# Kernel optimization log

Hardware: AMD Instinct MI355X
Metric: run time of the kernel (lower is better)

## Reference

```python
import jax, jax.numpy as jnp
import numpy as np

N_NODES = 50000
N_EDGES = 800000
IN_CH = 128
HEADS = 4
OUT_CH = 4
N_GRAPHS = 64
NEG_SLOPE = 0.2  # GATv2Conv default leaky_relu slope
EPS = 1e-5       # GraphNorm eps


def _seg_sum(x, seg, n):
    return jax.ops.segment_sum(x, seg, num_segments=n)


def _seg_mean(x, seg, n):
    s = _seg_sum(x, seg, n)
    cnt = _seg_sum(jnp.ones((seg.shape[0],), x.dtype), seg, n)
    return s / jnp.maximum(cnt, 1.0)[:, None]


def gatv2_conv(x, src, dst, n, w_l, w_r, att, bias, heads, out_ch, concat):
    # x: [N, F_in]; src/dst: [E_tot] (self-loops already appended)
    x_l = (x @ w_l).reshape(n, heads, out_ch)
    x_r = (x @ w_r).reshape(n, heads, out_ch)
    m = jax.nn.leaky_relu(x_l[src] + x_r[dst], NEG_SLOPE)   # [E, H, C]
    e = jnp.einsum('ehc,hc->eh', m, att)                    # [E, H]
    # softmax over incoming edges of each destination node
    e_max = jax.ops.segment_max(e, dst, num_segments=n)     # [N, H]
    w = jnp.exp(e - e_max[dst])
    denom = _seg_sum(w, dst, n)                             # [N, H]
    alpha = w / denom[dst]
    out = _seg_sum(alpha[:, :, None] * x_l[src], dst, n)    # [N, H, C]
    out = out.reshape(n, heads * out_ch) if concat else out.mean(axis=1)
    return out + bias


def graph_norm(x, batch, weight, bias, mean_scale, n_graphs):
    mu = _seg_mean(x, batch, n_graphs)                      # [G, C]
    out = x - mu[batch] * mean_scale
    var = _seg_mean(out * out, batch, n_graphs)
    return out / jnp.sqrt(var[batch] + EPS) * weight + bias


def setup_inputs() -> dict:
    key = jax.random.key(0)
    ks = jax.random.split(key, 20)
    H = HEADS
    d = {}
    d['x'] = jax.random.normal(ks[0], (N_NODES, IN_CH), dtype=jnp.float32)
    d['edge_index'] = jax.random.randint(ks[1], (2, N_EDGES), 0, N_NODES, dtype=jnp.int32)
    d['batch'] = jnp.sort(jax.random.randint(ks[2], (N_NODES,), 0, N_GRAPHS, dtype=jnp.int32))
    def glorot(k, shape):
        fan = shape[0] + shape[-1]
        return jax.random.normal(k, shape, dtype=jnp.float32) * np.sqrt(2.0 / fan).astype(np.float32)
    # layer 1: in 128 -> 32 per head, concat -> 128
    d['w_l1'] = glorot(ks[3], (IN_CH, H * 32)); d['w_r1'] = glorot(ks[4], (IN_CH, H * 32))
    d['att1'] = glorot(ks[5], (H, 32)); d['b1'] = jnp.zeros((H * 32,), jnp.float32)
    d['gn1_w'] = jnp.ones((H * 32,), jnp.float32); d['gn1_b'] = jnp.zeros((H * 32,), jnp.float32); d['gn1_s'] = jnp.ones((H * 32,), jnp.float32)
    # layer 2: 128 -> 16 per head, concat -> 64
    d['w_l2'] = glorot(ks[6], (H * 32, H * 16)); d['w_r2'] = glorot(ks[7], (H * 32, H * 16))
    d['att2'] = glorot(ks[8], (H, 16)); d['b2'] = jnp.zeros((H * 16,), jnp.float32)
    d['gn2_w'] = jnp.ones((H * 16,), jnp.float32); d['gn2_b'] = jnp.zeros((H * 16,), jnp.float32); d['gn2_s'] = jnp.ones((H * 16,), jnp.float32)
    # layer 3: 64 -> 8 per head, mean over heads -> 8
    d['w_l3'] = glorot(ks[9], (H * 16, H * 8)); d['w_r3'] = glorot(ks[10], (H * 16, H * 8))
    d['att3'] = glorot(ks[11], (H, 8)); d['b3'] = jnp.zeros((8,), jnp.float32)
    d['gn3_w'] = jnp.ones((8,), jnp.float32); d['gn3_b'] = jnp.zeros((8,), jnp.float32); d['gn3_s'] = jnp.ones((8,), jnp.float32)
    d['lin_w'] = glorot(ks[12], (8, OUT_CH)); d['lin_b'] = jnp.zeros((OUT_CH,), jnp.float32)
    return d


def reference(x, edge_index, batch,
              w_l1, w_r1, att1, b1, gn1_w, gn1_b, gn1_s,
              w_l2, w_r2, att2, b2, gn2_w, gn2_b, gn2_s,
              w_l3, w_r3, att3, b3, gn3_w, gn3_b, gn3_s,
              lin_w, lin_b):
    n = x.shape[0]
    loop = jnp.arange(n, dtype=edge_index.dtype)
    src = jnp.concatenate([edge_index[0], loop])  # add_self_loops=True (PyG default)
    dst = jnp.concatenate([edge_index[1], loop])
    h = gatv2_conv(x, src, dst, n, w_l1, w_r1, att1, b1, HEADS, 32, True)
    h = jax.nn.relu(graph_norm(h, batch, gn1_w, gn1_b, gn1_s, N_GRAPHS))
    h = gatv2_conv(h, src, dst, n, w_l2, w_r2, att2, b2, HEADS, 16, True)
    h = jax.nn.relu(graph_norm(h, batch, gn2_w, gn2_b, gn2_s, N_GRAPHS))
    h = gatv2_conv(h, src, dst, n, w_l3, w_r3, att3, b3, HEADS, 8, False)
    h = jax.nn.relu(graph_norm(h, batch, gn3_w, gn3_b, gn3_s, N_GRAPHS))
    features = _seg_mean(h, batch, N_GRAPHS)  # global_mean_pool -> [G, 8]
    logits = features @ lin_w + lin_b         # [G, OUT_CH]
    return (logits, features)
```

## Files before the change

### kernel.cpp

```cpp
#include <hip/hip_runtime.h>
#include <hip/hip_fp16.h>
#include <math.h>

#define NN 50000
#define NE 800000
#define ET (NE + NN)
#define NG 64
#define H 4
#define NBK 196
#define CH 4096
#define SB ((ET + CH - 1) / CH)

typedef _Float16 half8 __attribute__((ext_vector_type(8)));
typedef _Float16 hv2 __attribute__((ext_vector_type(2)));
typedef float floatx4 __attribute__((ext_vector_type(4)));


template <int K, int M2>
__device__ __forceinline__ void wprep_fn(int chunk, const float* __restrict__ Wl, const float* __restrict__ Wr,
                                         _Float16* __restrict__ Wfrag) {
    constexpr int MTOT = 2 * M2, NT = MTOT / 16;
    if (chunk >= MTOT * K / 8) return;
    int lane = chunk & 63, tt = chunk >> 6;
    int t = tt % NT, kt = tt / NT;
    int n = t * 16 + (lane & 15);
    int kb = kt * 32 + (lane >> 4) * 8;
    const float* src = (n < M2) ? (Wl + n) : (Wr + (n - M2));
    half8 h;
#pragma unroll
    for (int j = 0; j < 8; ++j) h[j] = (_Float16)src[(size_t)(kb + j) * M2];
    *(half8*)(Wfrag + (size_t)chunk * 8) = h;
}


__global__ __launch_bounds__(256) void k_prep(const float* __restrict__ Wl1, const float* __restrict__ Wr1,
                                              const float* __restrict__ Wl2, const float* __restrict__ Wr2,
                                              const float* __restrict__ Wl3, const float* __restrict__ Wr3,
                                              _Float16* __restrict__ Wf1, _Float16* __restrict__ Wf2,
                                              _Float16* __restrict__ Wf3,
                                              const int* __restrict__ batch, int* __restrict__ bpos,
                                              const int* __restrict__ ei, int* __restrict__ bcnt) {
    int b = blockIdx.x, t = threadIdx.x;
    if (b < 16) { wprep_fn<128, 128>(b * 256 + t, Wl1, Wr1, Wf1); return; }
    if (b < 24) { wprep_fn<128, 64>((b - 16) * 256 + t, Wl2, Wr2, Wf2); return; }
    if (b < 26) { wprep_fn<64, 32>((b - 24) * 256 + t, Wl3, Wr3, Wf3); return; }
    if (b < 26 + NBK) {
        int i = (b - 26) * 256 + t;
        if (i >= NN) return;
        int cur = batch[i];
        int prev = (i == 0) ? -1 : batch[i - 1];
        for (int g = prev + 1; g <= cur; ++g) bpos[g] = i;
        if (i == NN - 1)
            for (int g = cur + 1; g <= NG; ++g) bpos[g] = NN;
        return;
    }
    __shared__ int hist[NBK];
    int b0 = b - 26 - NBK;
    for (int i = t; i < NBK; i += 256) hist[i] = 0;
    __syncthreads();
#pragma unroll
    for (int pass = 0; pass < CH / 256; ++pass) {
        int e = b0 * CH + pass * 256 + t;
        if (e < ET) {
            int d = (e < NE) ? ei[NE + e] : (e - NE);
            atomicAdd(&hist[d >> 8], 1);
        }
    }
    __syncthreads();
    if (t < NBK) bcnt[t * SB + b0] = hist[t];
}


__global__ __launch_bounds__(256) void k_bscanA(const int* __restrict__ bcnt, int* __restrict__ boff,
                                                int* __restrict__ tot) {
    __shared__ int lds[256];
    int b = blockIdx.x, t = threadIdx.x;
    int v = (t < SB) ? bcnt[b * SB + t] : 0;
    lds[t] = v;
    __syncthreads();
    for (int off = 1; off < 256; off <<= 1) {
        int y = (t >= off) ? lds[t - off] : 0;
        __syncthreads();
        lds[t] += y;
        __syncthreads();
    }
    if (t < SB) boff[b * SB + t] = lds[t] - v;
    if (t == 255) tot[b] = lds[255];
}


__device__ __forceinline__ void edge_sd(int e, const int* __restrict__ ei, int& s, int& d) {
    if (e < NE) { s = ei[e]; d = ei[NE + e]; } else { s = e - NE; d = s; }
}

__global__ __launch_bounds__(256) void k_bscatter(const int* __restrict__ ei, const int* __restrict__ tot,
                                                  const int* __restrict__ boff, unsigned int* __restrict__ ebuf) {
    __shared__ int eb[256];
    __shared__ int cur[NBK];
    int b0 = blockIdx.x, t = threadIdx.x;
    int v = (t < NBK) ? tot[t] : 0;
    eb[t] = v;
    __syncthreads();
    for (int off = 1; off < 256; off <<= 1) {
        int y = (t >= off) ? eb[t - off] : 0;
        __syncthreads();
        eb[t] += y;
        __syncthreads();
    }
    if (t < NBK) cur[t] = (eb[t] - v) + boff[t * SB + b0];
    __syncthreads();
#pragma unroll
    for (int pass = 0; pass < CH / 256; ++pass) {
        int e = b0 * CH + pass * 256 + t;
        if (e < ET) {
            int s, d;
            edge_sd(e, ei, s, d);
            int pos = atomicAdd(&cur[d >> 8], 1);
            ebuf[pos] = ((unsigned)s << 16) | (unsigned)(d & 255);
        }
    }
}


__global__ __launch_bounds__(256) void k_bsort(const unsigned int* __restrict__ ebuf,
                                               const int* __restrict__ tot,
                                               int* __restrict__ rowptr, unsigned short* __restrict__ colsrc) {
    __shared__ int eb[256];
    __shared__ int sbase;
    __shared__ int cnt2[256];
    __shared__ int sc[256];
    __shared__ int cur2[256];
    int b = blockIdx.x, t = threadIdx.x;
    int v = (t < NBK) ? tot[t] : 0;
    eb[t] = v;
    __syncthreads();
    for (int off = 1; off < 256; off <<= 1) {
        int y = (t >= off) ? eb[t - off] : 0;
        __syncthreads();
        eb[t] += y;
        __syncthreads();
    }
    if (t == b) sbase = eb[t] - v;
    __syncthreads();
    int base = sbase, n = tot[b];
    cnt2[t] = 0;
    __syncthreads();
    for (int i = t; i < n; i += 256) atomicAdd(&cnt2[ebuf[base + i] & 255], 1);
    __syncthreads();
    int cv = cnt2[t];
    sc[t] = cv;
    __syncthreads();
    for (int off = 1; off < 256; off <<= 1) {
        int y = (t >= off) ? sc[t - off] : 0;
        __syncthreads();
        sc[t] += y;
        __syncthreads();
    }
    int excl = sc[t] - cv;
    int d = b * 256 + t;
    if (d < NN) rowptr[d] = base + excl;
    if (b == 0 && t == 0) rowptr[NN] = ET;
    cur2[t] = excl;
    __syncthreads();
    for (int i = t; i < n; i += 256) {
        unsigned u = ebuf[base + i];
        int pos = atomicAdd(&cur2[u & 255], 1);
        colsrc[base + pos] = (unsigned short)(u >> 16);
    }
}


template <typename AT>
__device__ __forceinline__ half8 load_a8(const AT* __restrict__ ap) {
    if constexpr (__is_same(AT, _Float16)) {
        return *(const half8*)ap;
    } else {
        const float4* p = (const float4*)ap;
        float4 a = p[0], b = p[1];
        half8 h;
        h[0] = (_Float16)a.x; h[1] = (_Float16)a.y; h[2] = (_Float16)a.z; h[3] = (_Float16)a.w;
        h[4] = (_Float16)b.x; h[5] = (_Float16)b.y; h[6] = (_Float16)b.z; h[7] = (_Float16)b.w;
        return h;
    }
}

template <int K, int M2, typename AT>
__global__ __launch_bounds__(256) void k_dualgemm(const AT* __restrict__ Ain,
                                                  const _Float16* __restrict__ Wfrag,
                                                  __half* __restrict__ Ol, float* __restrict__ Or) {
    constexpr int MTOT = 2 * M2;
    constexpr int NT = MTOT / 16;
    constexpr int KT = K / 32;
    int tid = threadIdx.x;
    int wid = tid >> 6, lane = tid & 63;
    int q = lane >> 4, l15 = lane & 15;
    int r0 = blockIdx.x * 64 + wid * 16;
    int arow = min(r0 + l15, NN - 1);
    const AT* ap = Ain + (size_t)arow * K + q * 8;

    floatx4 acc[NT];
#pragma unroll
    for (int t = 0; t < NT; ++t) acc[t] = (floatx4){0.f, 0.f, 0.f, 0.f};

#pragma unroll
    for (int kt = 0; kt < KT; ++kt) {
        half8 a8 = load_a8<AT>(ap + kt * 32);
        const _Float16* wp = Wfrag + ((size_t)(kt * NT) * 64 + lane) * 8;
#pragma unroll
        for (int t = 0; t < NT; ++t) {
            half8 b8 = *(const half8*)(wp + (size_t)t * 64 * 8);
            acc[t] = __builtin_amdgcn_mfma_f32_16x16x32_f16(a8, b8, acc[t], 0, 0, 0);
        }
    }

#pragma unroll
    for (int t = 0; t < NT; ++t) {
        int cn = t * 16 + l15;
#pragma unroll
        for (int reg = 0; reg < 4; ++reg) {
            int r = r0 + q * 4 + reg;
            if (r < NN) {
                if (cn < M2) Ol[(size_t)r * M2 + cn] = __float2half(acc[t][reg]);
                else         Or[(size_t)r * M2 + (cn - M2)] = acc[t][reg];
            }
        }
    }
}


template <int CP> struct HVec { hv2 h2[CP / 2]; };

template <int CP>
__device__ __forceinline__ HVec<CP> load_hv(const __half* __restrict__ p) {
    HVec<CP> r;
    if constexpr (CP == 8) { float4 t = *(const float4*)p; r = *(HVec<CP>*)&t; }
    else if constexpr (CP == 4) { float2 t = *(const float2*)p; r = *(HVec<CP>*)&t; }
    else { r.h2[0] = *(const hv2*)p; }
    return r;
}

template <int C, int EP, bool CONCAT>
__global__ __launch_bounds__(256, 8) void k_attn(const __half* __restrict__ xl, const float* __restrict__ xr,
                                                 const int* __restrict__ rowptr,
                                                 const unsigned short* __restrict__ colsrc,
                                                 const float* __restrict__ att, const float* __restrict__ bias,
                                                 float* __restrict__ out) {
    constexpr int CP = C / EP;
    constexpr int LEP = (EP == 4) ? 2 : ((EP == 2) ? 1 : 0);
    int t = blockIdx.x * 256 + threadIdx.x;
    int part = t & (EP - 1);
    int nh = t >> LEP;
    if (nh >= NN * H) return;
    int node = nh >> 2, h = nh & 3;
    int cbase = h * C + part * CP;
    hv2 xrr2[CP / 2], attv2[CP / 2];
    float acc[CP];
    {
        const float* p = xr + (size_t)node * (H * C) + cbase;
        const float* q = att + cbase;
#pragma unroll
        for (int j = 0; j < CP / 2; ++j) {
            xrr2[j] = (hv2){(_Float16)p[2 * j], (_Float16)p[2 * j + 1]};
            attv2[j] = (hv2){(_Float16)q[2 * j], (_Float16)q[2 * j + 1]};
        }
#pragma unroll
        for (int c = 0; c < CP; ++c) acc[c] = 0.f;
    }
    float denom = 0.f;
    int beg = rowptr[node], end = rowptr[node + 1];

    auto process = [&](const HVec<CP>& xv) {
        float part_s = 0.f;
#pragma unroll
        for (int j = 0; j < CP / 2; ++j) {
            hv2 z = xv.h2[j] + xrr2[j];
            hv2 l = __builtin_elementwise_max(z, z * (_Float16)0.2f);
            part_s = __builtin_amdgcn_fdot2(l, attv2[j], part_s, false);
        }
        float score = part_s;
#pragma unroll
        for (int mask = 1; mask < EP; mask <<= 1) score += __shfl_xor(score, mask, 64);
        float w = __expf(score);
        denom += w;
        const _Float16* xh = (const _Float16*)&xv;
#pragma unroll
        for (int c = 0; c < CP; ++c) acc[c] = fmaf(w, (float)xh[c], acc[c]);
    };

    int idx = beg;
    for (; idx + 4 <= end; idx += 4) {
        int s0 = colsrc[idx], s1 = colsrc[idx + 1], s2 = colsrc[idx + 2], s3 = colsrc[idx + 3];
        HVec<CP> xv0 = load_hv<CP>(xl + (size_t)s0 * (H * C) + cbase);
        HVec<CP> xv1 = load_hv<CP>(xl + (size_t)s1 * (H * C) + cbase);
        HVec<CP> xv2 = load_hv<CP>(xl + (size_t)s2 * (H * C) + cbase);
        HVec<CP> xv3 = load_hv<CP>(xl + (size_t)s3 * (H * C) + cbase);
        process(xv0);
        process(xv1);
        process(xv2);
        process(xv3);
    }
    for (; idx < end; ++idx) {
        int s = colsrc[idx];
        HVec<CP> xv = load_hv<CP>(xl + (size_t)s * (H * C) + cbase);
        process(xv);
    }

    float inv = 1.f / denom;
    float* op = out + (size_t)node * (H * C) + cbase;
    float v[CP];
#pragma unroll
    for (int c = 0; c < CP; ++c) {
        v[c] = acc[c] * inv;
        if (CONCAT) v[c] += bias[cbase + c];
    }
    if constexpr (CP == 8) {
        *(float4*)(op) = make_float4(v[0], v[1], v[2], v[3]);
        *(float4*)(op + 4) = make_float4(v[4], v[5], v[6], v[7]);
    } else if constexpr (CP == 4) {
        *(float4*)(op) = make_float4(v[0], v[1], v[2], v[3]);
    } else {
        *(float2*)(op) = make_float2(v[0], v[1]);
    }
}


template <int LOGC, int SPLIT>
__global__ __launch_bounds__(256) void k_gnred2(const float* __restrict__ h, const int* __restrict__ bpos,
                                                float* __restrict__ sum, float* __restrict__ sumsq) {
    constexpr int C = 1 << LOGC;
    constexpr int RG = 256 >> LOGC;
    int g = blockIdx.x / SPLIT, s = blockIdx.x % SPLIT;
    int c = threadIdx.x & (C - 1);
    int rg = threadIdx.x >> LOGC;
    int b0 = bpos[g], b1 = bpos[g + 1];
    int n = b1 - b0;
    int seg = (n + SPLIT - 1) / SPLIT;
    int r0 = b0 + s * seg;
    int r1 = min(r0 + seg, b1);
    float sv = 0.f, ssv = 0.f;
    for (int r = r0 + rg; r < r1; r += RG) {
        float x = h[(size_t)r * C + c];
        sv += x; ssv += x * x;
    }
    __shared__ float ls[256], lss[256];
    ls[threadIdx.x] = sv; lss[threadIdx.x] = ssv;
    __syncthreads();
    for (int off = 128; off >= C; off >>= 1) {
        if (threadIdx.x < off) {
            ls[threadIdx.x] += ls[threadIdx.x + off];
            lss[threadIdx.x] += lss[threadIdx.x + off];
        }
        __syncthreads();
    }
    if (threadIdx.x < C) {
        atomicAdd(&sum[g * C + threadIdx.x], ls[threadIdx.x]);
        atomicAdd(&sumsq[g * C + threadIdx.x], lss[threadIdx.x]);
    }
}

__global__ __launch_bounds__(256) void k_gnnorm(float* __restrict__ h, const int* __restrict__ batch,
                                                const float* __restrict__ sum, const float* __restrict__ sumsq,
                                                const int* __restrict__ bpos, const float* __restrict__ w,
                                                const float* __restrict__ b, const float* __restrict__ ms,
                                                int logC, __half* __restrict__ h16) {
    int C = 1 << logC;
    int i = blockIdx.x * 256 + threadIdx.x;
    if (i >= NN * C) return;
    int nd = i >> logC, c = i & (C - 1);
    int g = batch[nd];
    float cg = fmaxf((float)(bpos[g + 1] - bpos[g]), 1.f);
    float mu = sum[g * C + c] / cg;
    float ex2 = sumsq[g * C + c] / cg;
    float s_ = ms[c];
    float var = ex2 - (2.f * s_ - s_ * s_) * mu * mu;
    float y = (h[i] - mu * s_) * rsqrtf(var + 1e-5f) * w[c] + b[c];
    y = fmaxf(y, 0.f);
    if (h16) h16[i] = __float2half(y);
    else     h[i] = y;
}


template <int SPLIT>
__global__ __launch_bounds__(256) void k_headgn(const float* __restrict__ tmp, const float* __restrict__ b3,
                                                const int* __restrict__ bpos, float* __restrict__ Af,
                                                float* __restrict__ sum, float* __restrict__ sumsq) {
    constexpr int C = 8, RG = 32;
    int g = blockIdx.x / SPLIT, s = blockIdx.x % SPLIT;
    int c = threadIdx.x & 7;
    int rg = threadIdx.x >> 3;
    int b0 = bpos[g], b1 = bpos[g + 1];
    int n = b1 - b0;
    int seg = (n + SPLIT - 1) / SPLIT;
    int r0 = b0 + s * seg;
    int r1 = min(r0 + seg, b1);
    float bias = b3[c];
    float sv = 0.f, ssv = 0.f;
    for (int r = r0 + rg; r < r1; r += RG) {
        const float* p = tmp + (size_t)r * 32 + c;
        float v = 0.25f * (p[0] + p[8] + p[16] + p[24]) + bias;
        Af[(size_t)r * C + c] = v;
        sv += v; ssv += v * v;
    }
    __shared__ float ls[256], lss[256];
    ls[threadIdx.x] = sv; lss[threadIdx.x] = ssv;
    __syncthreads();
    for (int off = 128; off >= C; off >>= 1) {
        if (threadIdx.x < off) {
            ls[threadIdx.x] += ls[threadIdx.x + off];
            lss[threadIdx.x] += lss[threadIdx.x + off];
        }
        __syncthreads();
    }
    if (threadIdx.x < C) {
        atomicAdd(&sum[g * C + threadIdx.x], ls[threadIdx.x]);
        atomicAdd(&sumsq[g * C + threadIdx.x], lss[threadIdx.x]);
    }
}


template <int SPLIT>
__global__ __launch_bounds__(256) void k_gnpool(const float* __restrict__ Af, const int* __restrict__ bpos,
                                                const float* __restrict__ sum, const float* __restrict__ sumsq,
                                                const float* __restrict__ w,
                                                const float* __restrict__ b, const float* __restrict__ ms,
                                                float* __restrict__ pool) {
    constexpr int C = 8, RG = 32;
    int g = blockIdx.x / SPLIT, s = blockIdx.x % SPLIT;
    int c = threadIdx.x & 7;
    int rg = threadIdx.x >> 3;
    int b0 = bpos[g], b1 = bpos[g + 1];
    int n = b1 - b0;
    int seg = (n + SPLIT - 1) / SPLIT;
    int r0 = b0 + s * seg;
    int r1 = min(r0 + seg, b1);
    float cg = fmaxf((float)n, 1.f);
    float mu = sum[g * C + c] / cg;
    float ex2 = sumsq[g * C + c] / cg;
    float s_ = ms[c];
    float var = ex2 - (2.f * s_ - s_ * s_) * mu * mu;
    float rs = rsqrtf(var + 1e-5f) * w[c];
    float bb = b[c], mus = mu * s_;
    float pv = 0.f;
    for (int r = r0 + rg; r < r1; r += RG) {
        float y = fmaxf((Af[(size_t)r * C + c] - mus) * rs + bb, 0.f);
        pv += y;
    }
    __shared__ float ls[256];
    ls[threadIdx.x] = pv;
    __syncthreads();
    for (int off = 128; off >= C; off >>= 1) {
        if (threadIdx.x < off) ls[threadIdx.x] += ls[threadIdx.x + off];
        __syncthreads();
    }
    if (threadIdx.x < C) atomicAdd(&pool[g * C + threadIdx.x], ls[threadIdx.x]);
}


__global__ __launch_bounds__(512) void k_final(const float* __restrict__ pool, const int* __restrict__ bpos,
                                               const float* __restrict__ lw, const float* __restrict__ lb,
                                               float* __restrict__ outp) {
    __shared__ float feat[512];
    int t = threadIdx.x;
    int g = t >> 3;
    float f = pool[t] / fmaxf((float)(bpos[g + 1] - bpos[g]), 1.f);
    feat[t] = f;
    outp[256 + t] = f;
    __syncthreads();
    if (t < 256) {
        int g2 = t >> 2, o = t & 3;
        float a = lb[o];
#pragma unroll
        for (int cc = 0; cc < 8; ++cc) a += feat[g2 * 8 + cc] * lw[cc * 4 + o];
        outp[t] = a;
    }
}


extern "C" void kernel_launch(void* const* d_in, const int* in_sizes, int n_in,
                              void* d_out, int out_size, void* d_ws, size_t ws_size,
                              hipStream_t stream) {
    const float* x    = (const float*)d_in[0];
    const int*   ei   = (const int*)d_in[1];
    const int*   batch= (const int*)d_in[2];
    const float *w_l1 = (const float*)d_in[3],  *w_r1 = (const float*)d_in[4];
    const float *att1 = (const float*)d_in[5],  *b1   = (const float*)d_in[6];
    const float *gn1w = (const float*)d_in[7],  *gn1b = (const float*)d_in[8],  *gn1s = (const float*)d_in[9];
    const float *w_l2 = (const float*)d_in[10], *w_r2 = (const float*)d_in[11];
    const float *att2 = (const float*)d_in[12], *b2   = (const float*)d_in[13];
    const float *gn2w = (const float*)d_in[14], *gn2b = (const float*)d_in[15], *gn2s = (const float*)d_in[16];
    const float *w_l3 = (const float*)d_in[17], *w_r3 = (const float*)d_in[18];
    const float *att3 = (const float*)d_in[19], *b3   = (const float*)d_in[20];
    const float *gn3w = (const float*)d_in[21], *gn3b = (const float*)d_in[22], *gn3s = (const float*)d_in[23];
    const float *lw   = (const float*)d_in[24], *lb   = (const float*)d_in[25];

    char* ws = (char*)d_ws;
    size_t off = 0;
    auto alloc = [&](size_t bytes) -> void* {
        void* p = ws + off;
        off += (bytes + 255) & ~(size_t)255;
        return p;
    };
    __half* Ah  = (__half*)alloc((size_t)NN * 128 * 2);
    __half* Xh  = (__half*)alloc((size_t)NN * 128 * 2);
    float*  B   = (float*)alloc((size_t)NN * 128 * 4);
    float*  Cb  = (float*)alloc((size_t)NN * 64 * 4);
    float*  Af  = (float*)alloc((size_t)NN * 8 * 4);
    _Float16* Wf1 = (_Float16*)alloc((size_t)256 * 128 * 2);
    _Float16* Wf2 = (_Float16*)alloc((size_t)128 * 128 * 2);
    _Float16* Wf3 = (_Float16*)alloc((size_t)64 * 64 * 2);
    int* rowptr = (int*)alloc((size_t)(NN + 1) * 4);
    unsigned short* colsrc = (unsigned short*)alloc((size_t)ET * 2);
    unsigned int* ebuf = (unsigned int*)alloc((size_t)ET * 4);
    int* bcnt   = (int*)alloc((size_t)NBK * SB * 4);
    int* boff   = (int*)alloc((size_t)NBK * SB * 4);
    int* tot    = (int*)alloc((size_t)NBK * 4);
    int* bpos   = (int*)alloc((size_t)(NG + 1) * 4);
    char* zbase = ws + off;
    float* sum1 = (float*)alloc((size_t)NG * 128 * 4);
    float* sq1  = (float*)alloc((size_t)NG * 128 * 4);
    float* sum2 = (float*)alloc((size_t)NG * 64 * 4);
    float* sq2  = (float*)alloc((size_t)NG * 64 * 4);
    float* sum3 = (float*)alloc((size_t)NG * 8 * 4);
    float* sq3  = (float*)alloc((size_t)NG * 8 * 4);
    float* pool = (float*)alloc((size_t)NG * 8 * 4);
    size_t zbytes = (size_t)((ws + off) - zbase);
    (void)hipMemsetAsync(zbase, 0, zbytes, stream);

    k_prep<<<26 + NBK + SB, 256, 0, stream>>>(w_l1, w_r1, w_l2, w_r2, w_l3, w_r3, Wf1, Wf2, Wf3,
                                              batch, bpos, ei, bcnt);
    k_bscanA<<<NBK, 256, 0, stream>>>(bcnt, boff, tot);
    k_bscatter<<<SB, 256, 0, stream>>>(ei, tot, boff, ebuf);
    k_bsort<<<NBK, 256, 0, stream>>>(ebuf, tot, rowptr, colsrc);

    int gA1 = (NN * H * 4) / 256;
    int gA2 = (NN * H * 2 + 255) / 256;
    int gA3 = (NN * H + 255) / 256;
    int gD  = (NN + 63) / 64;

    k_dualgemm<128, 128, float><<<gD, 256, 0, stream>>>(x, Wf1, Ah, B);
    k_attn<32, 4, true><<<gA1, 256, 0, stream>>>(Ah, B, rowptr, colsrc, att1, b1, B);
    k_gnred2<7, 8><<<NG * 8, 256, 0, stream>>>(B, bpos, sum1, sq1);
    k_gnnorm<<<(NN * 128 + 255) / 256, 256, 0, stream>>>(B, batch, sum1, sq1, bpos, gn1w, gn1b, gn1s, 7, Xh);

    k_dualgemm<128, 64, _Float16><<<gD, 256, 0, stream>>>((const _Float16*)Xh, Wf2, Ah, Cb);
    k_attn<16, 2, true><<<gA2, 256, 0, stream>>>(Ah, Cb, rowptr, colsrc, att2, b2, Cb);
    k_gnred2<6, 8><<<NG * 8, 256, 0, stream>>>(Cb, bpos, sum2, sq2);
    k_gnnorm<<<(NN * 64 + 255) / 256, 256, 0, stream>>>(Cb, batch, sum2, sq2, bpos, gn2w, gn2b, gn2s, 6, Xh);

    k_dualgemm<64, 32, _Float16><<<gD, 256, 0, stream>>>((const _Float16*)Xh, Wf3, Ah, B);
    k_attn<8, 1, false><<<gA3, 256, 0, stream>>>(Ah, B, rowptr, colsrc, att3, nullptr, B);
    k_headgn<8><<<NG * 8, 256, 0, stream>>>(B, b3, bpos, Af, sum3, sq3);
    k_gnpool<8><<<NG * 8, 256, 0, stream>>>(Af, bpos, sum3, sq3, gn3w, gn3b, gn3s, pool);
    k_final<<<1, 512, 0, stream>>>(pool, bpos, lw, lb, (float*)d_out);
}
```

Before: 324.6 us.

## Fuse layer-1 GEMM with bucket scan, halve chunk size, widen attn per-thread channels

Merges the first dual GEMM with the bucket-offset scan into a single launch, which removes one kernel launch and lets the independent GEMM and scan work share the GPU. It halves the edge chunk size (CH), so the scan now handles two entries per thread. Layer-1 attention moves from 4 to 2 threads per node-head with 16 channels each, and its occupancy hint in launch bounds is dropped. The trade-off is more registers and wider loads per thread in the attention kernel, plus more chunk blocks in the sort pipeline.

Result: no change. 323.4 us (-0.4%).

```diff
diff --git a/kernel.cpp b/kernel.cpp
--- a/kernel.cpp
+++ b/kernel.cpp
@@ -8,8 +8,9 @@
 #define NG 64
 #define H 4
 #define NBK 196
-#define CH 4096
+#define CH 2048
 #define SB ((ET + CH - 1) / CH)
+#define GD ((NN + 63) / 64)
 
 typedef _Float16 half8 __attribute__((ext_vector_type(8)));
 typedef _Float16 hv2 __attribute__((ext_vector_type(2)));
@@ -71,12 +72,78 @@
 }
 
 
-__global__ __launch_bounds__(256) void k_bscanA(const int* __restrict__ bcnt, int* __restrict__ boff,
-                                                int* __restrict__ tot) {
+template <typename AT>
+__device__ __forceinline__ half8 load_a8(const AT* __restrict__ ap) {
+    if constexpr (__is_same(AT, _Float16)) {
+        return *(const half8*)ap;
+    } else {
+        const float4* p = (const float4*)ap;
+        float4 a = p[0], b = p[1];
+        half8 h;
+        h[0] = (_Float16)a.x; h[1] = (_Float16)a.y; h[2] = (_Float16)a.z; h[3] = (_Float16)a.w;
+        h[4] = (_Float16)b.x; h[5] = (_Float16)b.y; h[6] = (_Float16)b.z; h[7] = (_Float16)b.w;
+        return h;
+    }
+}
+
+template <int K, int M2, typename AT>
+__device__ __forceinline__ void dualgemm_body(int blk, int tid, const AT* __restrict__ Ain,
+                                              const _Float16* __restrict__ Wfrag,
+                                              __half* __restrict__ Ol, float* __restrict__ Or) {
+    constexpr int MTOT = 2 * M2;
+    constexpr int NT = MTOT / 16;
+    constexpr int KT = K / 32;
+    int wid = tid >> 6, lane = tid & 63;
+    int q = lane >> 4, l15 = lane & 15;
+    int r0 = blk * 64 + wid * 16;
+    int arow = min(r0 + l15, NN - 1);
+    const AT* ap = Ain + (size_t)arow * K + q * 8;
+
+    floatx4 acc[NT];
+#pragma unroll
+    for (int t = 0; t < NT; ++t) acc[t] = (floatx4){0.f, 0.f, 0.f, 0.f};
+
+#pragma unroll
+    for (int kt = 0; kt < KT; ++kt) {
+        half8 a8 = load_a8<AT>(ap + kt * 32);
+        const _Float16* wp = Wfrag + ((size_t)(kt * NT) * 64 + lane) * 8;
+#pragma unroll
+        for (int t = 0; t < NT; ++t) {
+            half8 b8 = *(const half8*)(wp + (size_t)t * 64 * 8);
+            acc[t] = __builtin_amdgcn_mfma_f32_16x16x32_f16(a8, b8, acc[t], 0, 0, 0);
+        }
+    }
+
+#pragma unroll
+    for (int t = 0; t < NT; ++t) {
+        int cn = t * 16 + l15;
+#pragma unroll
+        for (int reg = 0; reg < 4; ++reg) {
+            int r = r0 + q * 4 + reg;
+            if (r < NN) {
+                if (cn < M2) Ol[(size_t)r * M2 + cn] = __float2half(acc[t][reg]);
+                else         Or[(size_t)r * M2 + (cn - M2)] = acc[t][reg];
+            }
+        }
+    }
+}
+
+template <int K, int M2, typename AT>
+__global__ __launch_bounds__(256) void k_dualgemm(const AT* __restrict__ Ain,
+                                                  const _Float16* __restrict__ Wfrag,
+                                                  __half* __restrict__ Ol, float* __restrict__ Or) {
+    dualgemm_body<K, M2, AT>(blockIdx.x, threadIdx.x, Ain, Wfrag, Ol, Or);
+}
+
+
+__device__ __forceinline__ void bscanA_fn(int b, int t, const int* __restrict__ bcnt,
+                                          int* __restrict__ boff, int* __restrict__ tot) {
     __shared__ int lds[256];
-    int b = blockIdx.x, t = threadIdx.x;
-    int v = (t < SB) ? bcnt[b * SB + t] : 0;
-    lds[t] = v;
+    int i0 = 2 * t, i1 = 2 * t + 1;
+    int v0 = (i0 < SB) ? bcnt[b * SB + i0] : 0;
+    int v1 = (i1 < SB) ? bcnt[b * SB + i1] : 0;
+    int pair = v0 + v1;
+    lds[t] = pair;
     __syncthreads();
     for (int off = 1; off < 256; off <<= 1) {
         int y = (t >= off) ? lds[t - off] : 0;
@@ -84,8 +151,19 @@
         lds[t] += y;
         __syncthreads();
     }
-    if (t < SB) boff[b * SB + t] = lds[t] - v;
+    int excl = lds[t] - pair;
+    if (i0 < SB) boff[b * SB + i0] = excl;
+    if (i1 < SB) boff[b * SB + i1] = excl + v0;
     if (t == 255) tot[b] = lds[255];
+}
+
+
+__global__ __launch_bounds__(256) void k_gemm1_scan(const float* __restrict__ x, const _Float16* __restrict__ Wf1,
+                                                    __half* __restrict__ Ol, float* __restrict__ Or,
+                                                    const int* __restrict__ bcnt, int* __restrict__ boff,
+                                                    int* __restrict__ tot) {
+    if (blockIdx.x < GD) dualgemm_body<128, 128, float>(blockIdx.x, threadIdx.x, x, Wf1, Ol, Or);
+    else                 bscanA_fn(blockIdx.x - GD, threadIdx.x, bcnt, boff, tot);
 }
 
 
@@ -170,81 +248,31 @@
 }
 
 
-template <typename AT>
-__device__ __forceinline__ half8 load_a8(const AT* __restrict__ ap) {
-    if constexpr (__is_same(AT, _Float16)) {
-        return *(const half8*)ap;
-    } else {
-        const float4* p = (const float4*)ap;
-        float4 a = p[0], b = p[1];
-        half8 h;
-        h[0] = (_Float16)a.x; h[1] = (_Float16)a.y; h[2] = (_Float16)a.z; h[3] = (_Float16)a.w;
-        h[4] = (_Float16)b.x; h[5] = (_Float16)b.y; h[6] = (_Float16)b.z; h[7] = (_Float16)b.w;
-        return h;
-    }
-}
-
-template <int K, int M2, typename AT>
-__global__ __launch_bounds__(256) void k_dualgemm(const AT* __restrict__ Ain,
-                                                  const _Float16* __restrict__ Wfrag,
-                                                  __half* __restrict__ Ol, float* __restrict__ Or) {
-    constexpr int MTOT = 2 * M2;
-    constexpr int NT = MTOT / 16;
-    constexpr int KT = K / 32;
-    int tid = threadIdx.x;
-    int wid = tid >> 6, lane = tid & 63;
-    int q = lane >> 4, l15 = lane & 15;
-    int r0 = blockIdx.x * 64 + wid * 16;
-    int arow = min(r0 + l15, NN - 1);
-    const AT* ap = Ain + (size_t)arow * K + q * 8;
-
-    floatx4 acc[NT];
-#pragma unroll
-    for (int t = 0; t < NT; ++t) acc[t] = (floatx4){0.f, 0.f, 0.f, 0.f};
-
-#pragma unroll
-    for (int kt = 0; kt < KT; ++kt) {
-        half8 a8 = load_a8<AT>(ap + kt * 32);
-        const _Float16* wp = Wfrag + ((size_t)(kt * NT) * 64 + lane) * 8;
-#pragma unroll
-        for (int t = 0; t < NT; ++t) {
-            half8 b8 = *(const half8*)(wp + (size_t)t * 64 * 8);
-            acc[t] = __builtin_amdgcn_mfma_f32_16x16x32_f16(a8, b8, acc[t], 0, 0, 0);
-        }
-    }
-
-#pragma unroll
-    for (int t = 0; t < NT; ++t) {
-        int cn = t * 16 + l15;
-#pragma unroll
-        for (int reg = 0; reg < 4; ++reg) {
-            int r = r0 + q * 4 + reg;
-            if (r < NN) {
-                if (cn < M2) Ol[(size_t)r * M2 + cn] = __float2half(acc[t][reg]);
-                else         Or[(size_t)r * M2 + (cn - M2)] = acc[t][reg];
-            }
-        }
-    }
-}
-
-
 template <int CP> struct HVec { hv2 h2[CP / 2]; };
 
 template <int CP>
 __device__ __forceinline__ HVec<CP> load_hv(const __half* __restrict__ p) {
     HVec<CP> r;
-    if constexpr (CP == 8) { float4 t = *(const float4*)p; r = *(HVec<CP>*)&t; }
-    else if constexpr (CP == 4) { float2 t = *(const float2*)p; r = *(HVec<CP>*)&t; }
-    else { r.h2[0] = *(const hv2*)p; }
+    if constexpr (CP == 16) {
+        float4* rp = (float4*)&r;
+        rp[0] = ((const float4*)p)[0];
+        rp[1] = ((const float4*)p)[1];
+    } else if constexpr (CP == 8) {
+        float4 t = *(const float4*)p; r = *(HVec<CP>*)&t;
+    } else if constexpr (CP == 4) {
+        float2 t = *(const float2*)p; r = *(HVec<CP>*)&t;
+    } else {
+        r.h2[0] = *(const hv2*)p;
+    }
     return r;
 }
 
 template <int C, int EP, bool CONCAT>
-__global__ __launch_bounds__(256, 8) void k_attn(const __half* __restrict__ xl, const float* __restrict__ xr,
-                                                 const int* __restrict__ rowptr,
-                                                 const unsigned short* __restrict__ colsrc,
-                                                 const float* __restrict__ att, const float* __restrict__ bias,
-                                                 float* __restrict__ out) {
+__global__ __launch_bounds__(256) void k_attn(const __half* __restrict__ xl, const float* __restrict__ xr,
+                                              const int* __restrict__ rowptr,
+                                              const unsigned short* __restrict__ colsrc,
+                                              const float* __restrict__ att, const float* __restrict__ bias,
+                                              float* __restrict__ out) {
     constexpr int CP = C / EP;
     constexpr int LEP = (EP == 4) ? 2 : ((EP == 2) ? 1 : 0);
     int t = blockIdx.x * 256 + threadIdx.x;
@@ -313,7 +341,11 @@
         v[c] = acc[c] * inv;
         if (CONCAT) v[c] += bias[cbase + c];
     }
-    if constexpr (CP == 8) {
+    if constexpr (CP == 16) {
+#pragma unroll
+        for (int j = 0; j < 4; ++j)
+            *(float4*)(op + 4 * j) = make_float4(v[4 * j], v[4 * j + 1], v[4 * j + 2], v[4 * j + 3]);
+    } else if constexpr (CP == 8) {
         *(float4*)(op) = make_float4(v[0], v[1], v[2], v[3]);
         *(float4*)(op + 4) = make_float4(v[4], v[5], v[6], v[7]);
     } else if constexpr (CP == 4) {
@@ -416,7 +448,6 @@
         atomicAdd(&sumsq[g * C + threadIdx.x], lss[threadIdx.x]);
     }
 }
-
 
 template <int SPLIT>
 __global__ __launch_bounds__(256) void k_gnpool(const float* __restrict__ Af, const int* __restrict__ bpos,
@@ -528,26 +559,24 @@
 
     k_prep<<<26 + NBK + SB, 256, 0, stream>>>(w_l1, w_r1, w_l2, w_r2, w_l3, w_r3, Wf1, Wf2, Wf3,
                                               batch, bpos, ei, bcnt);
-    k_bscanA<<<NBK, 256, 0, stream>>>(bcnt, boff, tot);
+    k_gemm1_scan<<<GD + NBK, 256, 0, stream>>>(x, Wf1, Ah, B, bcnt, boff, tot);
     k_bscatter<<<SB, 256, 0, stream>>>(ei, tot, boff, ebuf);
     k_bsort<<<NBK, 256, 0, stream>>>(ebuf, tot, rowptr, colsrc);
 
-    int gA1 = (NN * H * 4) / 256;
+    int gA1 = (NN * H * 2 + 255) / 256;
     int gA2 = (NN * H * 2 + 255) / 256;
     int gA3 = (NN * H + 255) / 256;
-    int gD  = (NN + 63) / 64;
-
-    k_dualgemm<128, 128, float><<<gD, 256, 0, stream>>>(x, Wf1, Ah, B);
-    k_attn<32, 4, true><<<gA1, 256, 0, stream>>>(Ah, B, rowptr, colsrc, att1, b1, B);
+
+    k_attn<32, 2, true><<<gA1, 256, 0, stream>>>(Ah, B, rowptr, colsrc, att1, b1, B);
     k_gnred2<7, 8><<<NG * 8, 256, 0, stream>>>(B, bpos, sum1, sq1);
     k_gnnorm<<<(NN * 128 + 255) / 256, 256, 0, stream>>>(B, batch, sum1, sq1, bpos, gn1w, gn1b, gn1s, 7, Xh);
 
-    k_dualgemm<128, 64, _Float16><<<gD, 256, 0, stream>>>((const _Float16*)Xh, Wf2, Ah, Cb);
+    k_dualgemm<128, 64, _Float16><<<GD, 256, 0, stream>>>((const _Float16*)Xh, Wf2, Ah, Cb);
     k_attn<16, 2, true><<<gA2, 256, 0, stream>>>(Ah, Cb, rowptr, colsrc, att2, b2, Cb);
     k_gnred2<6, 8><<<NG * 8, 256, 0, stream>>>(Cb, bpos, sum2, sq2);
     k_gnnorm<<<(NN * 64 + 255) / 256, 256, 0, stream>>>(Cb, batch, sum2, sq2, bpos, gn2w, gn2b, gn2s, 6, Xh);
 
-    k_dualgemm<64, 32, _Float16><<<gD, 256, 0, stream>>>((const _Float16*)Xh, Wf3, Ah, B);
+    k_dualgemm<64, 32, _Float16><<<GD, 256, 0, stream>>>((const _Float16*)Xh, Wf3, Ah, B);
     k_attn<8, 1, false><<<gA3, 256, 0, stream>>>(Ah, B, rowptr, colsrc, att3, nullptr, B);
     k_headgn<8><<<NG * 8, 256, 0, stream>>>(B, b3, bpos, Af, sum3, sq3);
     k_gnpool<8><<<NG * 8, 256, 0, stream>>>(Af, bpos, sum3, sq3, gn3w, gn3b, gn3s, pool);
```
